# Kernel tuning notes

Measured on AMD Instinct MI355X. Metric: run time of the kernel, lower is better.

Reference implementation:

```python
import jax, jax.numpy as jnp
import numpy as np

N_ACTIVE = 200000   # active voxels
GRID = 96           # spatial grid extent per axis
C = 128             # inplanes == outplanes
EPS = 1e-4          # scn BatchNormalization default eps


def _build_rulebook(n, g, seed=0):
    """Submanifold 3x3x3 rulebook: for each of 27 offsets, pairs (in_site, out_site)
    where coord[in] = coord[out] + offset and both sites are active. Padded to
    length n with dummy index n."""
    rng = np.random.default_rng(seed)
    lin = rng.choice(g ** 3, size=n, replace=False)
    coords = np.stack(np.unravel_index(lin, (g, g, g)), axis=1)  # [n,3]
    lut = -np.ones(g ** 3, dtype=np.int64)
    lut[lin] = np.arange(n)
    in_rows, out_rows = [], []
    for dx in (-1, 0, 1):
        for dy in (-1, 0, 1):
            for dz in (-1, 0, 1):
                nb = coords + np.array([dx, dy, dz])
                valid = np.all((nb >= 0) & (nb < g), axis=1)
                j = np.full(n, -1, dtype=np.int64)
                j[valid] = lut[np.ravel_multi_index(nb[valid].T, (g, g, g))]
                hit = j >= 0
                ii = j[hit]
                oi = np.nonzero(hit)[0].astype(np.int64)
                pad = n - ii.shape[0]
                in_rows.append(np.concatenate([ii, np.full(pad, n, dtype=np.int64)]))
                out_rows.append(np.concatenate([oi, np.full(pad, n, dtype=np.int64)]))
    return np.stack(in_rows), np.stack(out_rows)  # each [27, n]


def setup_inputs() -> dict:
    key = jax.random.key(0)
    k_feat, k_w1, k_w2 = jax.random.split(key, 3)
    in_idx_np, out_idx_np = _build_rulebook(N_ACTIVE, GRID)
    w_std = 1.0 / np.sqrt(27 * C)
    return {
        "features": jax.random.normal(k_feat, (N_ACTIVE, C), dtype=jnp.float32),
        "W1": jax.random.normal(k_w1, (27, C, C), dtype=jnp.float32) * w_std,
        "gamma1": jnp.ones((C,), jnp.float32),
        "beta1": jnp.zeros((C,), jnp.float32),
        "W2": jax.random.normal(k_w2, (27, C, C), dtype=jnp.float32) * w_std,
        "gamma2": jnp.ones((C,), jnp.float32),
        "beta2": jnp.zeros((C,), jnp.float32),
        "in_idx": jnp.asarray(in_idx_np),
        "out_idx": jnp.asarray(out_idx_np),
    }


def _subm_conv(feats, W, in_idx, out_idx):
    # feats: [N, Cin]; W: [27, Cin, Cout]; rulebook idx: [27, K] (dummy = N)
    n, c_in = feats.shape
    c_out = W.shape[-1]
    feats_pad = jnp.concatenate([feats, jnp.zeros((1, c_in), feats.dtype)], axis=0)

    def step(acc, t):
        ii, oi, w = t
        contrib = feats_pad[ii] @ w  # [K, Cout] gather -> GEMM
        return acc.at[oi].add(contrib), None  # scatter-add (dummy row n absorbs pad)

    acc0 = jnp.zeros((n + 1, c_out), feats.dtype)
    acc, _ = jax.lax.scan(step, acc0, (in_idx, out_idx, W))
    return acc[:n]


def _bn(x, gamma, beta):
    # batch-norm over active sites (training-mode batch stats)
    m = x.mean(axis=0)
    v = x.var(axis=0)
    return (x - m) * jax.lax.rsqrt(v + EPS) * gamma + beta


def reference(features, W1, gamma1, beta1, W2, gamma2, beta2, in_idx, out_idx):
    out = _subm_conv(features, W1, in_idx, out_idx)
    out = jax.nn.relu(_bn(out, gamma1, beta1))          # scn.BatchNormReLU
    out = _subm_conv(out, W2, in_idx, out_idx)
    out = _bn(out, gamma2, beta2)                       # scn.BatchNormalization
    return jax.nn.relu(out + features)                  # AddTable + ReLU
```

## Files before the change

kernel.cpp:

```cpp
#include <hip/hip_runtime.h>

#define NACT 200000
#define MPAD 200064
#define NBLK 1563
#define KOFF 27

typedef __bf16 bf16x8 __attribute__((ext_vector_type(8)));
typedef __bf16 bf16x4 __attribute__((ext_vector_type(4)));
typedef float f32x4 __attribute__((ext_vector_type(4)));

__device__ __forceinline__ void async_load16(const void* g, void* l) {
  __builtin_amdgcn_global_load_lds(
      (__attribute__((address_space(1))) void*)g,
      (__attribute__((address_space(3))) void*)l, 16, 0, 0);
}

__global__ void fill_g(int* __restrict__ G) {
  int i = blockIdx.x * 256 + threadIdx.x;
  if (i < KOFF * MPAD) G[i] = NACT;
}

__global__ void scatter_g(const int* __restrict__ ii, const int* __restrict__ oi,
                          int* __restrict__ G) {
  int i = blockIdx.x * 256 + threadIdx.x;
  if (i >= KOFF * NACT) return;
  int k = i / NACT;
  int o = oi[i];
  G[k * MPAD + o] = ii[i];
}

__global__ void fix_g(int* __restrict__ G) {
  int k = threadIdx.x;
  if (k < KOFF) G[k * MPAD + NACT] = NACT;
}

__global__ void cast_feats(const float* __restrict__ F, __bf16* __restrict__ X) {
  int i = blockIdx.x * 256 + threadIdx.x;
  if (i >= (NACT + 1) * 32) return;
  float4 v = (i < NACT * 32) ? ((const float4*)F)[i] : make_float4(0.f, 0.f, 0.f, 0.f);
  bf16x4 o = {(__bf16)v.x, (__bf16)v.y, (__bf16)v.z, (__bf16)v.w};
  *(bf16x4*)(X + (i << 2)) = o;
}

__global__ void prep_w(const float* __restrict__ W1, const float* __restrict__ W2,
                       __bf16* __restrict__ T1, __bf16* __restrict__ T2) {
  int i = blockIdx.x * 256 + threadIdx.x;
  if (i >= KOFF * 128 * 128) return;
  int k = i >> 14, rem = i & 16383, n = rem >> 7, c = rem & 127;
  int src = (k << 14) + (c << 7) + n;
  T1[i] = (__bf16)W1[src];
  T2[i] = (__bf16)W2[src];
}

__global__ __launch_bounds__(256, 4) void gemm_gather(
    const __bf16* __restrict__ X,
    const __bf16* __restrict__ WT,
    const int* __restrict__ G,
    __bf16* __restrict__ Y,
    float* __restrict__ Pst)
{
  __shared__ __bf16 Alds[128 * 64];
  __shared__ __bf16 Blds[128 * 64];
  const int t = threadIdx.x;
  const int lane = t & 63;
  const int w = t >> 6;
  const int wm = (w & 1) << 6;
  const int wn = (w >> 1) << 6;
  const int m_base = blockIdx.x << 7;
  const int r0 = t >> 3;
  const int scb = t & 7;
  const int l15 = lane & 15;
  const int q4 = lane >> 4;

  f32x4 acc[4][4];
#pragma unroll
  for (int i = 0; i < 4; ++i)
#pragma unroll
    for (int j = 0; j < 4; ++j) acc[i][j] = (f32x4){0.f, 0.f, 0.f, 0.f};

  for (int kk = 0; kk < KOFF; ++kk) {
    int rowA[4];
#pragma unroll
    for (int j = 0; j < 4; ++j)
      rowA[j] = G[kk * MPAD + m_base + r0 + j * 32];
    const __bf16* wb = WT + (kk << 14);
#pragma unroll
    for (int s = 0; s < 2; ++s) {
      const int c0 = s << 6;
      __syncthreads();
#pragma unroll
      for (int j = 0; j < 4; ++j) {
        const int r = r0 + j * 32;
        const int gcb = scb ^ (r & 7);
        async_load16(wb + (r << 7) + c0 + (gcb << 3), &Blds[(((r << 3) + scb) << 3)]);
        async_load16(X + (rowA[j] << 7) + c0 + (gcb << 3), &Alds[(((r << 3) + scb) << 3)]);
      }
      __syncthreads();
#pragma unroll
      for (int ks = 0; ks < 2; ++ks) {
        bf16x8 af[4], bfr[4];
        const int cb0 = (ks << 2) + q4;
#pragma unroll
        for (int mi = 0; mi < 4; ++mi) {
          const int r = wm + mi * 16 + l15;
          af[mi] = *(const bf16x8*)&Alds[(((r << 3) + (cb0 ^ (r & 7))) << 3)];
        }
#pragma unroll
        for (int ni = 0; ni < 4; ++ni) {
          const int r = wn + ni * 16 + l15;
          bfr[ni] = *(const bf16x8*)&Blds[(((r << 3) + (cb0 ^ (r & 7))) << 3)];
        }
#pragma unroll
        for (int mi = 0; mi < 4; ++mi)
#pragma unroll
          for (int ni = 0; ni < 4; ++ni)
            acc[mi][ni] = __builtin_amdgcn_mfma_f32_16x16x32_bf16(
                af[mi], bfr[ni], acc[mi][ni], 0, 0, 0);
      }
    }
  }

#pragma unroll
  for (int mi = 0; mi < 4; ++mi) {
#pragma unroll
    for (int ni = 0; ni < 4; ++ni) {
      const int col = wn + ni * 16 + l15;
#pragma unroll
      for (int rg = 0; rg < 4; ++rg) {
        const int row = m_base + wm + mi * 16 + (q4 << 2) + rg;
        Y[(row << 7) + col] = (__bf16)acc[mi][ni][rg];
      }
    }
  }

  float s[4], s2[4];
#pragma unroll
  for (int ni = 0; ni < 4; ++ni) {
    float a = 0.f, b = 0.f;
#pragma unroll
    for (int mi = 0; mi < 4; ++mi)
#pragma unroll
      for (int rg = 0; rg < 4; ++rg) {
        float v = acc[mi][ni][rg];
        a += v; b += v * v;
      }
    s[ni] = a; s2[ni] = b;
  }
#pragma unroll
  for (int ni = 0; ni < 4; ++ni) {
    s[ni]  += __shfl_xor(s[ni], 16);  s[ni]  += __shfl_xor(s[ni], 32);
    s2[ni] += __shfl_xor(s2[ni], 16); s2[ni] += __shfl_xor(s2[ni], 32);
  }
  float* sc = (float*)Alds;
  __syncthreads();
  if (q4 == 0) {
#pragma unroll
    for (int ni = 0; ni < 4; ++ni) {
      sc[(w << 6) + ni * 16 + l15]       = s[ni];
      sc[256 + (w << 6) + ni * 16 + l15] = s2[ni];
    }
  }
  __syncthreads();
  {
    const int kind = t >> 7, col = t & 127;
    const int w1 = (col >> 6) << 1;
    const float v = sc[kind * 256 + (w1 << 6) + (col & 63)] +
                    sc[kind * 256 + ((w1 + 1) << 6) + (col & 63)];
    Pst[(size_t)t * NBLK + blockIdx.x] = v;
  }
}

__global__ void stats_reduce(const float* __restrict__ P, float* __restrict__ st) {
  int b = blockIdx.x;
  const float* p = P + (size_t)b * NBLK;
  float s = 0.f;
  for (int i = threadIdx.x; i < NBLK; i += 256) s += p[i];
  for (int off = 32; off; off >>= 1) s += __shfl_down(s, off);
  __shared__ float ls[4];
  if ((threadIdx.x & 63) == 0) ls[threadIdx.x >> 6] = s;
  __syncthreads();
  if (threadIdx.x == 0) st[b] = ls[0] + ls[1] + ls[2] + ls[3];
}

__global__ void bn_coeffs(const float* __restrict__ st, const float* __restrict__ gamma,
                          const float* __restrict__ beta, float* __restrict__ co) {
  int c = threadIdx.x;
  float m = st[c] * (1.f / NACT);
  float v = st[128 + c] * (1.f / NACT) - m * m;
  float sc = gamma[c] * rsqrtf(v + 1e-4f);
  co[c] = sc;
  co[128 + c] = beta[c] - m * sc;
}

__global__ void bn_relu_cast(const __bf16* __restrict__ Y, const float* __restrict__ co,
                             __bf16* __restrict__ X2) {
  int i = blockIdx.x * 256 + threadIdx.x;
  if (i >= (NACT + 1) * 16) return;
  bf16x8 o;
  if (i < NACT * 16) {
    bf16x8 v = ((const bf16x8*)Y)[i];
    int cg = (i & 15) << 3;
#pragma unroll
    for (int e = 0; e < 8; ++e) {
      float x = fmaf((float)v[e], co[cg + e], co[128 + cg + e]);
      o[e] = (__bf16)fmaxf(x, 0.f);
    }
  } else {
#pragma unroll
    for (int e = 0; e < 8; ++e) o[e] = (__bf16)0.f;
  }
  ((bf16x8*)X2)[i] = o;
}

__global__ void bn_add_relu(const __bf16* __restrict__ Y, const float* __restrict__ co,
                            const float* __restrict__ F, float* __restrict__ O) {
  int i = blockIdx.x * 256 + threadIdx.x;
  if (i >= NACT * 16) return;
  bf16x8 v = ((const bf16x8*)Y)[i];
  float4 f0 = ((const float4*)F)[2 * i];
  float4 f1 = ((const float4*)F)[2 * i + 1];
  int cg = (i & 15) << 3;
  float4 o0, o1;
  o0.x = fmaxf(fmaf((float)v[0], co[cg + 0], co[128 + cg + 0]) + f0.x, 0.f);
  o0.y = fmaxf(fmaf((float)v[1], co[cg + 1], co[128 + cg + 1]) + f0.y, 0.f);
  o0.z = fmaxf(fmaf((float)v[2], co[cg + 2], co[128 + cg + 2]) + f0.z, 0.f);
  o0.w = fmaxf(fmaf((float)v[3], co[cg + 3], co[128 + cg + 3]) + f0.w, 0.f);
  o1.x = fmaxf(fmaf((float)v[4], co[cg + 4], co[128 + cg + 4]) + f1.x, 0.f);
  o1.y = fmaxf(fmaf((float)v[5], co[cg + 5], co[128 + cg + 5]) + f1.y, 0.f);
  o1.z = fmaxf(fmaf((float)v[6], co[cg + 6], co[128 + cg + 6]) + f1.z, 0.f);
  o1.w = fmaxf(fmaf((float)v[7], co[cg + 7], co[128 + cg + 7]) + f1.w, 0.f);
  ((float4*)O)[2 * i] = o0;
  ((float4*)O)[2 * i + 1] = o1;
}

extern "C" void kernel_launch(void* const* d_in, const int* in_sizes, int n_in,
                              void* d_out, int out_size, void* d_ws, size_t ws_size,
                              hipStream_t stream) {
  const float* features = (const float*)d_in[0];
  const float* W1       = (const float*)d_in[1];
  const float* gamma1   = (const float*)d_in[2];
  const float* beta1    = (const float*)d_in[3];
  const float* W2       = (const float*)d_in[4];
  const float* gamma2   = (const float*)d_in[5];
  const float* beta2    = (const float*)d_in[6];
  const int* in_idx     = (const int*)d_in[7];
  const int* out_idx    = (const int*)d_in[8];

  char* ws = (char*)d_ws;
  size_t off = 0;
  int*    G   = (int*)(ws + off);    off += (size_t)KOFF * MPAD * 4;
  __bf16* X   = (__bf16*)(ws + off); off += (size_t)(NACT + 1) * 128 * 2;
  __bf16* T1  = (__bf16*)(ws + off); off += (size_t)KOFF * 128 * 128 * 2;
  __bf16* T2  = (__bf16*)(ws + off); off += (size_t)KOFF * 128 * 128 * 2;
  __bf16* Y   = (__bf16*)(ws + off); off += (size_t)MPAD * 128 * 2;
  float*  Pst = (float*)(ws + off);  off += (size_t)256 * NBLK * 4;
  float*  st  = (float*)(ws + off);  off += 4096;

  fill_g<<<(KOFF * MPAD + 255) / 256, 256, 0, stream>>>(G);
  scatter_g<<<(KOFF * NACT + 255) / 256, 256, 0, stream>>>(in_idx, out_idx, G);
  fix_g<<<1, 32, 0, stream>>>(G);
  cast_feats<<<((NACT + 1) * 32 + 255) / 256, 256, 0, stream>>>(features, X);
  prep_w<<<(KOFF * 128 * 128 + 255) / 256, 256, 0, stream>>>(W1, W2, T1, T2);

  gemm_gather<<<NBLK, 256, 0, stream>>>(X, T1, G, Y, Pst);
  stats_reduce<<<256, 256, 0, stream>>>(Pst, st);
  bn_coeffs<<<1, 128, 0, stream>>>(st, gamma1, beta1, st + 512);
  bn_relu_cast<<<((NACT + 1) * 16 + 255) / 256, 256, 0, stream>>>(Y, st + 512, X);

  gemm_gather<<<NBLK, 256, 0, stream>>>(X, T2, G, Y, Pst);
  stats_reduce<<<256, 256, 0, stream>>>(Pst, st);
  bn_coeffs<<<1, 128, 0, stream>>>(st, gamma2, beta2, st + 768);
  bn_add_relu<<<(NACT * 16 + 255) / 256, 256, 0, stream>>>(Y, st + 768, features, (float*)d_out);
}
```

Before: 609.9 us.

## Merge prep kernels, transpose gather map, fold BN stats into GEMM atomics

Fuses the rulebook scatter, feature cast and weight prep into one launch, and replaces the fill kernel with a memset. The gather table becomes row-major (site x offset, stride 32), and the next offset's index is prefetched one iteration ahead. The separate stats-reduce and BN-coefficient kernels are replaced by atomicAdd of per-block partial sums, with each elementwise thread recomputing its BN coefficients inline. The residual add now reads the bf16 copy of the features instead of the fp32 input, which saves bandwidth but adds rounding error and makes float atomics nondeterministic.

Result: slower. 771.5 us (+26.5%).

```diff
diff --git a/kernel.cpp b/kernel.cpp
--- a/kernel.cpp
+++ b/kernel.cpp
@@ -4,6 +4,11 @@
 #define MPAD 200064
 #define NBLK 1563
 #define KOFF 27
+#define GSTR 32
+
+#define SCAT_B 21094
+#define CAST_B 25001
+#define PREPW_B 1728
 
 typedef __bf16 bf16x8 __attribute__((ext_vector_type(8)));
 typedef __bf16 bf16x4 __attribute__((ext_vector_type(4)));
@@ -15,49 +20,44 @@
       (__attribute__((address_space(3))) void*)l, 16, 0, 0);
 }
 
-__global__ void fill_g(int* __restrict__ G) {
-  int i = blockIdx.x * 256 + threadIdx.x;
-  if (i < KOFF * MPAD) G[i] = NACT;
-}
-
-__global__ void scatter_g(const int* __restrict__ ii, const int* __restrict__ oi,
-                          int* __restrict__ G) {
-  int i = blockIdx.x * 256 + threadIdx.x;
-  if (i >= KOFF * NACT) return;
-  int k = i / NACT;
-  int o = oi[i];
-  G[k * MPAD + o] = ii[i];
-}
-
-__global__ void fix_g(int* __restrict__ G) {
-  int k = threadIdx.x;
-  if (k < KOFF) G[k * MPAD + NACT] = NACT;
-}
-
-__global__ void cast_feats(const float* __restrict__ F, __bf16* __restrict__ X) {
-  int i = blockIdx.x * 256 + threadIdx.x;
-  if (i >= (NACT + 1) * 32) return;
-  float4 v = (i < NACT * 32) ? ((const float4*)F)[i] : make_float4(0.f, 0.f, 0.f, 0.f);
-  bf16x4 o = {(__bf16)v.x, (__bf16)v.y, (__bf16)v.z, (__bf16)v.w};
-  *(bf16x4*)(X + (i << 2)) = o;
-}
-
-__global__ void prep_w(const float* __restrict__ W1, const float* __restrict__ W2,
-                       __bf16* __restrict__ T1, __bf16* __restrict__ T2) {
-  int i = blockIdx.x * 256 + threadIdx.x;
-  if (i >= KOFF * 128 * 128) return;
-  int k = i >> 14, rem = i & 16383, n = rem >> 7, c = rem & 127;
-  int src = (k << 14) + (c << 7) + n;
-  T1[i] = (__bf16)W1[src];
-  T2[i] = (__bf16)W2[src];
+__global__ void prep_all(const int* __restrict__ ii, const int* __restrict__ oi,
+                         int* __restrict__ G2,
+                         const float* __restrict__ F, __bf16* __restrict__ X,
+                         const float* __restrict__ W1, const float* __restrict__ W2,
+                         __bf16* __restrict__ T1, __bf16* __restrict__ T2,
+                         float* __restrict__ st) {
+  int b = blockIdx.x;
+  if (b < SCAT_B) {
+    int i = b * 256 + threadIdx.x;
+    if (i < KOFF * NACT) {
+      int o = oi[i];
+      if (o < NACT) G2[o * GSTR + (i / NACT)] = ii[i];
+    }
+  } else if (b < SCAT_B + CAST_B) {
+    int i = (b - SCAT_B) * 256 + threadIdx.x;
+    if (i < (NACT + 1) * 32) {
+      float4 v = (i < NACT * 32) ? ((const float4*)F)[i] : make_float4(0.f, 0.f, 0.f, 0.f);
+      bf16x4 o = {(__bf16)v.x, (__bf16)v.y, (__bf16)v.z, (__bf16)v.w};
+      *(bf16x4*)(X + (i << 2)) = o;
+    }
+  } else if (b < SCAT_B + CAST_B + PREPW_B) {
+    int i = (b - SCAT_B - CAST_B) * 256 + threadIdx.x;
+    int k = i >> 14, r = i & 16383, n = r >> 7, c = r & 127;
+    int src = (k << 14) + (c << 7) + n;
+    T1[i] = (__bf16)W1[src];
+    T2[i] = (__bf16)W2[src];
+  } else {
+    st[threadIdx.x] = 0.f;
+    st[256 + threadIdx.x] = 0.f;
+  }
 }
 
 __global__ __launch_bounds__(256, 4) void gemm_gather(
     const __bf16* __restrict__ X,
     const __bf16* __restrict__ WT,
-    const int* __restrict__ G,
+    const int* __restrict__ G2,
     __bf16* __restrict__ Y,
-    float* __restrict__ Pst)
+    float* __restrict__ st)
 {
   __shared__ __bf16 Alds[128 * 64];
   __shared__ __bf16 Blds[128 * 64];
@@ -78,11 +78,16 @@
 #pragma unroll
     for (int j = 0; j < 4; ++j) acc[i][j] = (f32x4){0.f, 0.f, 0.f, 0.f};
 
+  const int* gbase = G2 + (size_t)(m_base + r0) * GSTR;
+  int rowN[4];
+#pragma unroll
+  for (int j = 0; j < 4; ++j) rowN[j] = gbase[j * 32 * GSTR];
+
   for (int kk = 0; kk < KOFF; ++kk) {
     int rowA[4];
 #pragma unroll
     for (int j = 0; j < 4; ++j)
-      rowA[j] = G[kk * MPAD + m_base + r0 + j * 32];
+      rowA[j] = rowN[j] < NACT ? rowN[j] : NACT;
     const __bf16* wb = WT + (kk << 14);
 #pragma unroll
     for (int s = 0; s < 2; ++s) {
@@ -92,8 +97,12 @@
       for (int j = 0; j < 4; ++j) {
         const int r = r0 + j * 32;
         const int gcb = scb ^ (r & 7);
+        async_load16(X + (rowA[j] << 7) + c0 + (gcb << 3), &Alds[(((r << 3) + scb) << 3)]);
         async_load16(wb + (r << 7) + c0 + (gcb << 3), &Blds[(((r << 3) + scb) << 3)]);
-        async_load16(X + (rowA[j] << 7) + c0 + (gcb << 3), &Alds[(((r << 3) + scb) << 3)]);
+      }
+      if (s == 0 && kk + 1 < KOFF) {
+#pragma unroll
+        for (int j = 0; j < 4; ++j) rowN[j] = gbase[j * 32 * GSTR + kk + 1];
       }
       __syncthreads();
 #pragma unroll
@@ -166,43 +175,39 @@
     const int w1 = (col >> 6) << 1;
     const float v = sc[kind * 256 + (w1 << 6) + (col & 63)] +
                     sc[kind * 256 + ((w1 + 1) << 6) + (col & 63)];
-    Pst[(size_t)t * NBLK + blockIdx.x] = v;
-  }
-}
-
-__global__ void stats_reduce(const float* __restrict__ P, float* __restrict__ st) {
-  int b = blockIdx.x;
-  const float* p = P + (size_t)b * NBLK;
-  float s = 0.f;
-  for (int i = threadIdx.x; i < NBLK; i += 256) s += p[i];
-  for (int off = 32; off; off >>= 1) s += __shfl_down(s, off);
-  __shared__ float ls[4];
-  if ((threadIdx.x & 63) == 0) ls[threadIdx.x >> 6] = s;
-  __syncthreads();
-  if (threadIdx.x == 0) st[b] = ls[0] + ls[1] + ls[2] + ls[3];
-}
-
-__global__ void bn_coeffs(const float* __restrict__ st, const float* __restrict__ gamma,
-                          const float* __restrict__ beta, float* __restrict__ co) {
-  int c = threadIdx.x;
-  float m = st[c] * (1.f / NACT);
-  float v = st[128 + c] * (1.f / NACT) - m * m;
-  float sc = gamma[c] * rsqrtf(v + 1e-4f);
-  co[c] = sc;
-  co[128 + c] = beta[c] - m * sc;
-}
-
-__global__ void bn_relu_cast(const __bf16* __restrict__ Y, const float* __restrict__ co,
+    atomicAdd(&st[t], v);
+  }
+}
+
+__device__ __forceinline__ void bn_make(const float* __restrict__ st,
+                                        const float* __restrict__ gamma,
+                                        const float* __restrict__ beta,
+                                        int cg, float* sc, float* sh) {
+#pragma unroll
+  for (int e = 0; e < 8; ++e) {
+    int c = cg + e;
+    float m = st[c] * (1.f / NACT);
+    float v = st[128 + c] * (1.f / NACT) - m * m;
+    float s = gamma[c] * rsqrtf(v + 1e-4f);
+    sc[e] = s;
+    sh[e] = beta[c] - m * s;
+  }
+}
+
+__global__ void bn_relu_cast(const __bf16* __restrict__ Y, const float* __restrict__ st,
+                             const float* __restrict__ gamma, const float* __restrict__ beta,
                              __bf16* __restrict__ X2) {
   int i = blockIdx.x * 256 + threadIdx.x;
   if (i >= (NACT + 1) * 16) return;
   bf16x8 o;
   if (i < NACT * 16) {
+    int cg = (i & 15) << 3;
+    float sc[8], sh[8];
+    bn_make(st, gamma, beta, cg, sc, sh);
     bf16x8 v = ((const bf16x8*)Y)[i];
-    int cg = (i & 15) << 3;
 #pragma unroll
     for (int e = 0; e < 8; ++e) {
-      float x = fmaf((float)v[e], co[cg + e], co[128 + cg + e]);
+      float x = fmaf((float)v[e], sc[e], sh[e]);
       o[e] = (__bf16)fmaxf(x, 0.f);
     }
   } else {
@@ -212,23 +217,25 @@
   ((bf16x8*)X2)[i] = o;
 }
 
-__global__ void bn_add_relu(const __bf16* __restrict__ Y, const float* __restrict__ co,
-                            const float* __restrict__ F, float* __restrict__ O) {
+__global__ void bn_add_relu(const __bf16* __restrict__ Y, const float* __restrict__ st,
+                            const float* __restrict__ gamma, const float* __restrict__ beta,
+                            const __bf16* __restrict__ Xr, float* __restrict__ O) {
   int i = blockIdx.x * 256 + threadIdx.x;
   if (i >= NACT * 16) return;
+  int cg = (i & 15) << 3;
+  float sc[8], sh[8];
+  bn_make(st, gamma, beta, cg, sc, sh);
   bf16x8 v = ((const bf16x8*)Y)[i];
-  float4 f0 = ((const float4*)F)[2 * i];
-  float4 f1 = ((const float4*)F)[2 * i + 1];
-  int cg = (i & 15) << 3;
+  bf16x8 f = ((const bf16x8*)Xr)[i];
   float4 o0, o1;
-  o0.x = fmaxf(fmaf((float)v[0], co[cg + 0], co[128 + cg + 0]) + f0.x, 0.f);
-  o0.y = fmaxf(fmaf((float)v[1], co[cg + 1], co[128 + cg + 1]) + f0.y, 0.f);
-  o0.z = fmaxf(fmaf((float)v[2], co[cg + 2], co[128 + cg + 2]) + f0.z, 0.f);
-  o0.w = fmaxf(fmaf((float)v[3], co[cg + 3], co[128 + cg + 3]) + f0.w, 0.f);
-  o1.x = fmaxf(fmaf((float)v[4], co[cg + 4], co[128 + cg + 4]) + f1.x, 0.f);
-  o1.y = fmaxf(fmaf((float)v[5], co[cg + 5], co[128 + cg + 5]) + f1.y, 0.f);
-  o1.z = fmaxf(fmaf((float)v[6], co[cg + 6], co[128 + cg + 6]) + f1.z, 0.f);
-  o1.w = fmaxf(fmaf((float)v[7], co[cg + 7], co[128 + cg + 7]) + f1.w, 0.f);
+  o0.x = fmaxf(fmaf((float)v[0], sc[0], sh[0]) + (float)f[0], 0.f);
+  o0.y = fmaxf(fmaf((float)v[1], sc[1], sh[1]) + (float)f[1], 0.f);
+  o0.z = fmaxf(fmaf((float)v[2], sc[2], sh[2]) + (float)f[2], 0.f);
+  o0.w = fmaxf(fmaf((float)v[3], sc[3], sh[3]) + (float)f[3], 0.f);
+  o1.x = fmaxf(fmaf((float)v[4], sc[4], sh[4]) + (float)f[4], 0.f);
+  o1.y = fmaxf(fmaf((float)v[5], sc[5], sh[5]) + (float)f[5], 0.f);
+  o1.z = fmaxf(fmaf((float)v[6], sc[6], sh[6]) + (float)f[6], 0.f);
+  o1.w = fmaxf(fmaf((float)v[7], sc[7], sh[7]) + (float)f[7], 0.f);
   ((float4*)O)[2 * i] = o0;
   ((float4*)O)[2 * i + 1] = o1;
 }
@@ -248,27 +255,23 @@
 
   char* ws = (char*)d_ws;
   size_t off = 0;
-  int*    G   = (int*)(ws + off);    off += (size_t)KOFF * MPAD * 4;
-  __bf16* X   = (__bf16*)(ws + off); off += (size_t)(NACT + 1) * 128 * 2;
+  int*    G2  = (int*)(ws + off);    off += (size_t)MPAD * GSTR * 4;
+  __bf16* X1  = (__bf16*)(ws + off); off += (size_t)(NACT + 1) * 128 * 2;
+  __bf16* X2  = (__bf16*)(ws + off); off += (size_t)(NACT + 1) * 128 * 2;
   __bf16* T1  = (__bf16*)(ws + off); off += (size_t)KOFF * 128 * 128 * 2;
   __bf16* T2  = (__bf16*)(ws + off); off += (size_t)KOFF * 128 * 128 * 2;
   __bf16* Y   = (__bf16*)(ws + off); off += (size_t)MPAD * 128 * 2;
-  float*  Pst = (float*)(ws + off);  off += (size_t)256 * NBLK * 4;
   float*  st  = (float*)(ws + off);  off += 4096;
 
-  fill_g<<<(KOFF * MPAD + 255) / 256, 256, 0, stream>>>(G);
-  scatter_g<<<(KOFF * NACT + 255) / 256, 256, 0, stream>>>(in_idx, out_idx, G);
-  fix_g<<<1, 32, 0, stream>>>(G);
-  cast_feats<<<((NACT + 1) * 32 + 255) / 256, 256, 0, stream>>>(features, X);
-  prep_w<<<(KOFF * 128 * 128 + 255) / 256, 256, 0, stream>>>(W1, W2, T1, T2);
-
-  gemm_gather<<<NBLK, 256, 0, stream>>>(X, T1, G, Y, Pst);
-  stats_reduce<<<256, 256, 0, stream>>>(Pst, st);
-  bn_coeffs<<<1, 128, 0, stream>>>(st, gamma1, beta1, st + 512);
-  bn_relu_cast<<<((NACT + 1) * 16 + 255) / 256, 256, 0, stream>>>(Y, st + 512, X);
-
-  gemm_gather<<<NBLK, 256, 0, stream>>>(X, T2, G, Y, Pst);
-  stats_reduce<<<256, 256, 0, stream>>>(Pst, st);
-  bn_coeffs<<<1, 128, 0, stream>>>(st, gamma2, beta2, st + 768);
-  bn_add_relu<<<(NACT * 16 + 255) / 256, 256, 0, stream>>>(Y, st + 768, features, (float*)d_out);
-}
+  hipMemsetAsync(G2, 0x7F, (size_t)MPAD * GSTR * 4, stream);
+
+  prep_all<<<SCAT_B + CAST_B + PREPW_B + 1, 256, 0, stream>>>(
+      in_idx, out_idx, G2, features, X1, W1, W2, T1, T2, st);
+
+  gemm_gather<<<NBLK, 256, 0, stream>>>(X1, T1, G2, Y, st);
+  bn_relu_cast<<<((NACT + 1) * 16 + 255) / 256, 256, 0, stream>>>(Y, st, gamma1, beta1, X2);
+
+  gemm_gather<<<NBLK, 256, 0, stream>>>(X2, T2, G2, Y, st + 256);
+  bn_add_relu<<<(NACT * 16 + 255) / 256, 256, 0, stream>>>(Y, st + 256, gamma2, beta2,
+                                                           X1, (float*)d_out);
+}
```
